# Performance work log

Hardware: AMD Instinct MI355X
Metric: run time of the kernel (lower is better)

Reference implementation:

```python
import jax, jax.numpy as jnp
import numpy as np

B, S, D_MODEL, D_ATTN = 4, 2048, 1024, 1024
NEG_INF = jnp.float32(-jnp.inf)


def setup_inputs() -> dict:
    key = jax.random.key(0)
    ks = jax.random.split(key, 6)
    scale = 1.0 / np.sqrt(D_MODEL)
    return {
        "x": jax.random.normal(ks[0], (B, S, D_MODEL), dtype=jnp.float32),
        "mask": jnp.ones((B, S), dtype=jnp.float32),
        "Wq": jax.random.normal(ks[1], (D_ATTN, D_MODEL), dtype=jnp.float32) * scale,
        "Wk": jax.random.normal(ks[2], (D_ATTN, D_MODEL), dtype=jnp.float32) * scale,
        "Wv": jax.random.normal(ks[3], (D_ATTN, D_MODEL), dtype=jnp.float32) * scale,
        "Wo": jax.random.normal(ks[4], (D_MODEL, D_ATTN), dtype=jnp.float32) * scale,
        "bo": jnp.zeros((D_MODEL,), dtype=jnp.float32),
    }


def reference(x, mask, Wq, Wk, Wv, Wo, bo):
    # x: [B,S,Dm]; torch Linear weight is [out,in], so y = x @ W.T
    q = jnp.einsum("bsd,ad->bsa", x, Wq)  # [B,S,Da]
    k = jnp.einsum("bsd,ad->bsa", x, Wk)
    v = jnp.einsum("bsd,ad->bsa", x, Wv)  # NOTE: v from x (original quirk)
    logits = jnp.einsum("bqa,bka->bqk", q, k)  # [B,S,S]
    # causal mask (cross_attention=True path): keep lower triangle incl. diag
    causal = jnp.tril(jnp.ones((S, S), dtype=bool))
    logits = jnp.where(causal[None], logits, NEG_INF)
    # padding mask: outer product of per-token mask
    square_mask = mask[:, :, None] * mask[:, None, :]  # [B,S,S]
    logits = jnp.where(square_mask == 1, logits, NEG_INF)
    # scale by sqrt(d_model) AFTER masking (as in original)
    attn = jax.nn.softmax(logits / jnp.sqrt(jnp.float32(D_MODEL)), axis=-1)
    attn_out = jnp.einsum("bqk,bka->bqa", attn, v)  # [B,S,Da]
    return jnp.einsum("bsa,da->bsd", attn_out, Wo) + bo
```

## Files before the change

kernel.cpp:

```cpp
#include <hip/hip_runtime.h>
#include <hip/hip_bf16.h>
#include <cstdio>

typedef __bf16 bf16x8 __attribute__((ext_vector_type(8)));
typedef float f32x4 __attribute__((ext_vector_type(4)));

#define BM 128
#define BN 128
#define BK 64

__device__ __forceinline__ unsigned short f2bf(float f) {
  union { float f; unsigned u; } v; v.f = f;
  unsigned u = v.u;
  return (unsigned short)((u + 0x7FFFu + ((u >> 16) & 1u)) >> 16);
}

__device__ __forceinline__ float bf2f(unsigned short s) {
  union { unsigned u; float f; } v; v.u = ((unsigned)s) << 16;
  return v.f;
}

#define GLOAD16(gsrc, ldst) \
  __builtin_amdgcn_global_load_lds((const __attribute__((address_space(1))) void*)(gsrc), \
                                   (__attribute__((address_space(3))) void*)(ldst), 16, 0, 0)

#define SB_KLOOP(Ab, Bb)                                                        \
  for (int kt = 0; kt < 16; kt++) {                                             \
    const unsigned short* Ak = (Ab) + kt * BK;                                  \
    const unsigned short* Bk = (Bb) + kt * BK;                                  \
    _Pragma("unroll")                                                           \
    for (int r = 0; r < 4; r++) {                                               \
      int row = r * 32 + srow;                                                  \
      int sc = sch ^ (row & 7);                                                 \
      GLOAD16(Ak + (long)row * 1024 + sc * 8, &lds[0][(r * 32 + wave * 8) * BK]);\
    }                                                                           \
    _Pragma("unroll")                                                           \
    for (int r = 0; r < 4; r++) {                                               \
      int row = r * 32 + srow;                                                  \
      int sc = sch ^ (row & 7);                                                 \
      GLOAD16(Bk + (long)row * 1024 + sc * 8, &lds[1][(r * 32 + wave * 8) * BK]);\
    }                                                                           \
    __syncthreads();                                                            \
    _Pragma("unroll")                                                           \
    for (int s = 0; s < 2; s++) {                                               \
      bf16x8 av[4], bv[4];                                                      \
      _Pragma("unroll")                                                         \
      for (int i = 0; i < 4; i++) av[i] = *reinterpret_cast<const bf16x8*>(lds[0] + aOff[i][s]); \
      _Pragma("unroll")                                                         \
      for (int j = 0; j < 4; j++) bv[j] = *reinterpret_cast<const bf16x8*>(lds[1] + bOff[j][s]); \
      _Pragma("unroll")                                                         \
      for (int i = 0; i < 4; i++)                                               \
        _Pragma("unroll")                                                       \
        for (int j = 0; j < 4; j++)                                             \
          acc[i][j] = __builtin_amdgcn_mfma_f32_16x16x32_bf16(av[i], bv[j], acc[i][j], 0, 0, 0); \
    }                                                                           \
    __syncthreads();                                                            \
  }

#define SB_PREAMBLE                                                             \
  const int tid = threadIdx.x;                                                  \
  const int lane = tid & 63;                                                    \
  const int wave = tid >> 6;                                                    \
  const int wr = wave >> 1, wc = wave & 1;                                      \
  const int srow = tid >> 3;                                                    \
  const int sch = tid & 7;                                                      \
  (void)srow; (void)sch;                                                        \
  const f32x4 fzero = {0.f, 0.f, 0.f, 0.f};                                     \
  f32x4 acc[4][4];                                                              \
  _Pragma("unroll")                                                             \
  for (int i = 0; i < 4; i++)                                                   \
    _Pragma("unroll")                                                           \
    for (int j = 0; j < 4; j++) acc[i][j] = fzero;                              \
  int aOff[4][2], bOff[4][2];                                                   \
  _Pragma("unroll")                                                             \
  for (int i = 0; i < 4; i++) {                                                 \
    _Pragma("unroll")                                                           \
    for (int s = 0; s < 2; s++) {                                               \
      int ra = wr * 64 + i * 16 + (lane & 15);                                  \
      aOff[i][s] = ra * BK + (((s * 4 + (lane >> 4)) ^ (ra & 7)) * 8);          \
      int rb = wc * 64 + i * 16 + (lane & 15);                                  \
      bOff[i][s] = rb * BK + (((s * 4 + (lane >> 4)) ^ (rb & 7)) * 8);          \
    }                                                                           \
  }

__global__ __launch_bounds__(256)
void cast_ow(const float* __restrict__ Wo, const float* __restrict__ Wv,
             unsigned short* __restrict__ Wob, unsigned short* __restrict__ Wvt)
{
  __shared__ float t[64][65];
  const int blk = blockIdx.x;
  const int tid = threadIdx.x;
  if (blk < 512) {
    const int i = (blk * 256 + tid) * 8;
    float4 a = *reinterpret_cast<const float4*>(Wo + i);
    float4 b = *reinterpret_cast<const float4*>(Wo + i + 4);
    union { unsigned short us[8]; uint4 u4; } pk;
    pk.us[0] = f2bf(a.x); pk.us[1] = f2bf(a.y); pk.us[2] = f2bf(a.z); pk.us[3] = f2bf(a.w);
    pk.us[4] = f2bf(b.x); pk.us[5] = f2bf(b.y); pk.us[6] = f2bf(b.z); pk.us[7] = f2bf(b.w);
    *reinterpret_cast<uint4*>(Wob + i) = pk.u4;
    return;
  }
  const int tile = blk - 512;
  const int a0 = (tile >> 4) * 64;
  const int m0 = (tile & 15) * 64;
#pragma unroll
  for (int i = 0; i < 4; i++) {
    const int row = (tid >> 4) + i * 16;
    const int col4 = tid & 15;
    float4 f4 = *reinterpret_cast<const float4*>(Wv + (long)(a0 + row) * 1024 + m0 + col4 * 4);
    t[row][col4 * 4 + 0] = f4.x;
    t[row][col4 * 4 + 1] = f4.y;
    t[row][col4 * 4 + 2] = f4.z;
    t[row][col4 * 4 + 3] = f4.w;
  }
  __syncthreads();
#pragma unroll
  for (int j = 0; j < 2; j++) {
    const int mm = (tid >> 3) + j * 32;
    const int aa0 = (tid & 7) * 8;
    union { unsigned short us[8]; uint4 u4; } pk;
#pragma unroll
    for (int u = 0; u < 8; u++) pk.us[u] = f2bf(t[aa0 + u][mm]);
    *reinterpret_cast<uint4*>(Wvt + (long)(m0 + mm) * 1024 + a0 + aa0) = pk.u4;
  }
}

__global__ __launch_bounds__(256, 3)
void prep2(const float* __restrict__ x, const float* __restrict__ Wq,
           const float* __restrict__ Wk,
           const unsigned short* __restrict__ Wob, const unsigned short* __restrict__ Wvt,
           unsigned short* __restrict__ xb, unsigned short* __restrict__ Wqk,
           unsigned short* __restrict__ Wvo)
{
  __shared__ short lds[2][BM * BK];
  const int blk = blockIdx.x;

  if (blk >= 64) {
    const int tid = threadIdx.x;
    const float* src;
    unsigned short* dst;
    int i;
    if (blk < 4160) {
      src = x; dst = xb; i = ((blk - 64) * 256 + tid) * 8;
    } else {
      const int w = (blk - 4160) >> 9;
      const int off = (blk - 4160) & 511;
      src = (w == 0) ? Wq : Wk;
      dst = Wqk + (long)w * 1024 * 1024;
      i = (off * 256 + tid) * 8;
    }
    float4 a = *reinterpret_cast<const float4*>(src + i);
    float4 b = *reinterpret_cast<const float4*>(src + i + 4);
    union { unsigned short us[8]; uint4 u4; } pk;
    pk.us[0] = f2bf(a.x); pk.us[1] = f2bf(a.y); pk.us[2] = f2bf(a.z); pk.us[3] = f2bf(a.w);
    pk.us[4] = f2bf(b.x); pk.us[5] = f2bf(b.y); pk.us[6] = f2bf(b.z); pk.us[7] = f2bf(b.w);
    *reinterpret_cast<uint4*>(dst + i) = pk.u4;
    return;
  }

  const int t = blk;
  const int m0 = (t >> 3) * BM, n0 = (t & 7) * BN;
  const unsigned short* Ab = Wob + (long)m0 * 1024;
  const unsigned short* Bb = Wvt + (long)n0 * 1024;

  SB_PREAMBLE
  SB_KLOOP(Ab, Bb)

  const int rb4 = (lane >> 4) * 4;
  const int cl = lane & 15;
#pragma unroll
  for (int i = 0; i < 4; i++) {
#pragma unroll
    for (int j = 0; j < 4; j++) {
      const int gm = m0 + wr * 64 + i * 16 + rb4;
      const int gn = n0 + wc * 64 + j * 16 + cl;
#pragma unroll
      for (int r = 0; r < 4; r++)
        Wvo[(long)(gm + r) * 1024 + gn] = f2bf(acc[i][j][r]);
    }
  }
}

__global__ __launch_bounds__(256, 3)
void dispA2(const unsigned short* __restrict__ Xbf, const unsigned short* __restrict__ Wqk,
            const unsigned short* __restrict__ Wvo,
            unsigned short* __restrict__ Qb, unsigned short* __restrict__ Kb,
            unsigned short* __restrict__ VWt)
{
  __shared__ short lds[2][BM * BK];
  const int flat = blockIdx.x;
  const bool isQK = flat < 1024;
  int m0, n0;
  const unsigned short *Ab, *Bb;
  if (isQK) {
    const int swz = (flat & 7) * 128 + (flat >> 3);
    const int bx = swz & 15, by = swz >> 4;
    m0 = by * BM; n0 = bx * BN;
    Ab = Xbf + (long)m0 * 1024;
    Bb = Wqk + (long)n0 * 1024;
  } else {
    const int t = flat - 1024;
    const int swz = (t & 7) * 64 + (t >> 3);
    const int bx = swz & 7, by = swz >> 3;
    m0 = by * BM; n0 = bx * BN;
    Ab = Xbf + (long)m0 * 1024;
    Bb = Wvo + (long)n0 * 1024;
  }

  SB_PREAMBLE
  SB_KLOOP(Ab, Bb)

  const int rb4 = (lane >> 4) * 4;
  const int cl = lane & 15;
#pragma unroll
  for (int i = 0; i < 4; i++) {
#pragma unroll
    for (int j = 0; j < 4; j++) {
      const int gm = m0 + wr * 64 + i * 16 + rb4;
      const int gn = n0 + wc * 64 + j * 16 + cl;
      if (isQK) {
        if (gn < 1024) {
#pragma unroll
          for (int r = 0; r < 4; r++)
            Qb[(long)(gm + r) * 1024 + gn] = f2bf(acc[i][j][r]);
        } else {
#pragma unroll
          for (int r = 0; r < 4; r++)
            Kb[(long)(gm + r) * 1024 + (gn - 1024)] = f2bf(acc[i][j][r]);
        }
      } else {
        const int b = gm >> 11;
        const int sIdx = gm & 2047;
        unsigned short* C = VWt + (long)b * (2048L * 1024) + (long)gn * 2048 + sIdx;
        ushort4 pk;
        pk.x = f2bf(acc[i][j][0]);
        pk.y = f2bf(acc[i][j][1]);
        pk.z = f2bf(acc[i][j][2]);
        pk.w = f2bf(acc[i][j][3]);
        *reinterpret_cast<ushort4*>(C) = pk;
      }
    }
  }
}

__global__ __launch_bounds__(256, 3)
void dispS(const unsigned short* __restrict__ Qb, const unsigned short* __restrict__ Kb,
           unsigned short* __restrict__ Sb)
{
  __shared__ short lds[2][BM * BK];
  const int t = blockIdx.x;
  const int bz = t / 136;
  const int tt = t - bz * 136;
  const int swz = (tt & 7) * 17 + (tt >> 3);
  int i = (int)((sqrtf(8.f * (float)swz + 1.f) - 1.f) * 0.5f);
  while ((i + 1) * (i + 2) / 2 <= swz) ++i;
  while (i * (i + 1) / 2 > swz) --i;
  const int j = swz - i * (i + 1) / 2;
  const int m0 = i * BM, n0 = j * BN;
  const unsigned short* Ab = Qb + ((long)bz * 2048 + m0) * 1024;
  const unsigned short* Bb = Kb + ((long)bz * 2048 + n0) * 1024;

  SB_PREAMBLE
  SB_KLOOP(Ab, Bb)

  const int rb4 = (lane >> 4) * 4;
  const int cl = lane & 15;
  unsigned short* C = Sb + (long)bz * (2048L * 2048);
#pragma unroll
  for (int ii = 0; ii < 4; ii++) {
#pragma unroll
    for (int jj = 0; jj < 4; jj++) {
      const int gm = m0 + wr * 64 + ii * 16 + rb4;
      const int gn = n0 + wc * 64 + jj * 16 + cl;
#pragma unroll
      for (int r = 0; r < 4; r++)
        C[(long)(gm + r) * 2048 + gn] = f2bf(acc[ii][jj][r] * 0.03125f);
    }
  }
}

__global__ __launch_bounds__(256, 2)
void gemm_pv(const unsigned short* __restrict__ A, const unsigned short* __restrict__ B,
             float* __restrict__ Cv, const float* __restrict__ bias,
             int K, int ldA, int ldB, int ldC,
             long aBat, long bBat, long cBat)
{
  const int gx = gridDim.x;
  const int nwg = gx * gridDim.y;
  const int flat = blockIdx.y * gx + blockIdx.x;
  const int qch = nwg >> 3, rch = nwg & 7;
  const int xcd = flat & 7, idx = flat >> 3;
  const int swz = (xcd < rch ? xcd * (qch + 1) : rch * (qch + 1) + (xcd - rch) * qch) + idx;
  const int bx = swz % gx;
  const int bz = blockIdx.z;
  int by = swz / gx;
  if (bz >= 2) by = gridDim.y - 1 - by;

  const int m0 = by * BM;
  const int n0 = bx * BN;

  const unsigned short* Ab = A + (long)bz * aBat + (long)m0 * ldA;
  const unsigned short* Bb = B + (long)bz * bBat + (long)n0 * ldB;

  __shared__ short lds[2][2][BM * BK];

  const int tid = threadIdx.x;
  const int lane = tid & 63;
  const int wave = tid >> 6;
  const int wr = wave >> 1, wc = wave & 1;

  const int Keff = min(K, m0 + BM);
  const int nk = Keff / BK;

  const int srow = tid >> 3;
  const int sch = tid & 7;

  const f32x4 fzero = {0.f, 0.f, 0.f, 0.f};
  f32x4 acc[4][4];
#pragma unroll
  for (int i = 0; i < 4; i++)
#pragma unroll
    for (int j = 0; j < 4; j++) acc[i][j] = fzero;

  int aOff[4][2], bOff[4][2];
#pragma unroll
  for (int i = 0; i < 4; i++) {
#pragma unroll
    for (int s = 0; s < 2; s++) {
      int ra = wr * 64 + i * 16 + (lane & 15);
      aOff[i][s] = ra * BK + (((s * 4 + (lane >> 4)) ^ (ra & 7)) * 8);
      int rb = wc * 64 + i * 16 + (lane & 15);
      bOff[i][s] = rb * BK + (((s * 4 + (lane >> 4)) ^ (rb & 7)) * 8);
    }
  }

  auto stage = [&](int buf, int kt) {
    const unsigned short* Ak = Ab + kt * BK;
    const unsigned short* Bk = Bb + kt * BK;
#pragma unroll
    for (int r = 0; r < 4; r++) {
      int row = r * 32 + srow;
      int sc = sch ^ (row & 7);
      GLOAD16(Ak + (long)row * ldA + sc * 8, &lds[buf][0][(r * 32 + wave * 8) * BK]);
    }
#pragma unroll
    for (int r = 0; r < 4; r++) {
      int row = r * 32 + srow;
      int sc = sch ^ (row & 7);
      GLOAD16(Bk + (long)row * ldB + sc * 8, &lds[buf][1][(r * 32 + wave * 8) * BK]);
    }
  };

  stage(0, 0);
  stage(1, 1);
  asm volatile("s_waitcnt vmcnt(8)" ::: "memory");
  __builtin_amdgcn_sched_barrier(0);
  __builtin_amdgcn_s_barrier();

  int cur = 0;
  for (int kt = 0; kt < nk; kt++) {
    const short* La = lds[cur][0];
    const short* Lb = lds[cur][1];
    bf16x8 av[2][4], bv[2][4];
#pragma unroll
    for (int s = 0; s < 2; s++) {
#pragma unroll
      for (int i = 0; i < 4; i++) {
        av[s][i] = *reinterpret_cast<const bf16x8*>(La + aOff[i][s]);
        bv[s][i] = *reinterpret_cast<const bf16x8*>(Lb + bOff[i][s]);
      }
    }
    asm volatile("s_waitcnt lgkmcnt(0)" ::: "memory");
    __builtin_amdgcn_sched_barrier(0);
    __builtin_amdgcn_s_barrier();
    __builtin_amdgcn_sched_barrier(0);

    if (kt + 2 < nk) {
      stage(cur, kt + 2);
      asm volatile("s_waitcnt vmcnt(8)" ::: "memory");
    } else if (kt + 1 < nk) {
      asm volatile("s_waitcnt vmcnt(0)" ::: "memory");
    }
    if (kt + 1 < nk) {
      __builtin_amdgcn_s_barrier();
      __builtin_amdgcn_sched_barrier(0);
    }

    __builtin_amdgcn_s_setprio(1);
#pragma unroll
    for (int s = 0; s < 2; s++)
#pragma unroll
      for (int i = 0; i < 4; i++)
#pragma unroll
        for (int j = 0; j < 4; j++)
          acc[i][j] = __builtin_amdgcn_mfma_f32_16x16x32_bf16(av[s][i], bv[s][j], acc[i][j], 0, 0, 0);
    __builtin_amdgcn_s_setprio(0);
    __builtin_amdgcn_sched_barrier(0);
    cur ^= 1;
  }

  const int rb4 = (lane >> 4) * 4;
  const int cl = lane & 15;
#pragma unroll
  for (int i = 0; i < 4; i++) {
#pragma unroll
    for (int j = 0; j < 4; j++) {
      const int gm = m0 + wr * 64 + i * 16 + rb4;
      const int gn = n0 + wc * 64 + j * 16 + cl;
      float* C = Cv + (long)bz * cBat;
      const float bb = bias[gn];
#pragma unroll
      for (int r = 0; r < 4; r++)
        C[(long)(gm + r) * ldC + gn] = acc[i][j][r] + bb;
    }
  }
}

__global__ __launch_bounds__(256)
void softmax_rows(const unsigned short* __restrict__ Sb, const float* __restrict__ maskv,
                  unsigned short* __restrict__ P, int Sdim)
{
  const int wv = threadIdx.x >> 6;
  const int lane = threadIdx.x & 63;
  const int q = blockIdx.x * 4 + wv;
  const int b = blockIdx.y;
  const int kmax = (q & ~127) + 128;
  const unsigned short* row = Sb + ((long)b * Sdim + q) * Sdim;
  unsigned short* prow = P + ((long)b * Sdim + q) * Sdim;
  const float* mrow = maskv + (long)b * Sdim;
  const float mq = mrow[q];

  float v[4][8];
  float mx = -INFINITY;
#pragma unroll
  for (int c = 0; c < 4; c++) {
    const int k0 = c * 512 + lane * 8;
    if (c * 512 < kmax) {
      uint4 raw = *reinterpret_cast<const uint4*>(row + k0);
      const unsigned short* us = reinterpret_cast<const unsigned short*>(&raw);
      float4 ma = *reinterpret_cast<const float4*>(mrow + k0);
      float4 mb = *reinterpret_cast<const float4*>(mrow + k0 + 4);
      float mv[8] = {ma.x, ma.y, ma.z, ma.w, mb.x, mb.y, mb.z, mb.w};
#pragma unroll
      for (int u = 0; u < 8; u++) {
        const int k = k0 + u;
        const bool ok = (k <= q) && (mq * mv[u] == 1.0f);
        v[c][u] = ok ? bf2f(us[u]) : -INFINITY;
        mx = fmaxf(mx, v[c][u]);
      }
    } else {
#pragma unroll
      for (int u = 0; u < 8; u++) v[c][u] = -INFINITY;
    }
  }
#pragma unroll
  for (int o = 32; o; o >>= 1) mx = fmaxf(mx, __shfl_xor(mx, o));

  float sm = 0.f;
#pragma unroll
  for (int c = 0; c < 4; c++)
#pragma unroll
    for (int u = 0; u < 8; u++) {
      v[c][u] = (v[c][u] > -INFINITY) ? __expf(v[c][u] - mx) : 0.f;
      sm += v[c][u];
    }
#pragma unroll
  for (int o = 32; o; o >>= 1) sm += __shfl_xor(sm, o);
  const float inv = 1.0f / sm;

#pragma unroll
  for (int c = 0; c < 4; c++) {
    if (c * 512 < kmax) {
      union { unsigned short us[8]; uint4 u4; } pk;
#pragma unroll
      for (int u = 0; u < 8; u++) pk.us[u] = f2bf(v[c][u] * inv);
      *reinterpret_cast<uint4*>(prow + c * 512 + lane * 8) = pk.u4;
    }
  }
}

extern "C" void kernel_launch(void* const* d_in, const int* in_sizes, int n_in,
                              void* d_out, int out_size, void* d_ws, size_t ws_size,
                              hipStream_t stream)
{
  const int B = 4, S = 2048, D = 1024;
  const float* x  = (const float*)d_in[0];
  const float* mk = (const float*)d_in[1];
  const float* Wq = (const float*)d_in[2];
  const float* Wk = (const float*)d_in[3];
  const float* Wv = (const float*)d_in[4];
  const float* Wo = (const float*)d_in[5];
  const float* bo = (const float*)d_in[6];
  float* out = (float*)d_out;

  char* ws = (char*)d_ws;
  const long MB = 1024L * 1024L;
  unsigned short* Xbf  = (unsigned short*)(ws + 0);
  unsigned short* Qb   = (unsigned short*)(ws + 16 * MB);
  unsigned short* Kb   = (unsigned short*)(ws + 32 * MB);
  unsigned short* VWt  = (unsigned short*)(ws + 48 * MB);
  unsigned short* Wqk  = (unsigned short*)(ws + 64 * MB);
  unsigned short* Wvo  = (unsigned short*)(ws + 68 * MB);
  unsigned short* Wob  = (unsigned short*)(ws + 70 * MB);
  unsigned short* Sbuf = (unsigned short*)(ws + 72 * MB);
  unsigned short* Wvt  = Sbuf;
  unsigned short* P    = Qb;

  if (ws_size < (size_t)(104 * MB)) {
    fprintf(stderr, "kernel_launch: ws too small (%zu bytes, need 104MB)\n", ws_size);
    return;
  }

  cast_ow<<<dim3(768), dim3(256), 0, stream>>>(Wo, Wv, Wob, Wvt);
  prep2<<<dim3(5184), dim3(256), 0, stream>>>(x, Wq, Wk, Wob, Wvt, Xbf, Wqk, Wvo);
  dispA2<<<dim3(1536), dim3(256), 0, stream>>>(Xbf, Wqk, Wvo, Qb, Kb, VWt);
  dispS<<<dim3(544), dim3(256), 0, stream>>>(Qb, Kb, Sbuf);
  softmax_rows<<<dim3(512, 4), dim3(256), 0, stream>>>(Sbuf, mk, P, 2048);
  dim3 gO(1024 / BN, 2048 / BM, 4);
  gemm_pv<<<gO, dim3(256), 0, stream>>>(P, VWt, out, bo,
                                        2048, 2048, 2048, 1024,
                                        (long)S * S, (long)D * S, (long)S * D);
}
```

Before: 155.9 us.

## Fuse softmax into score epilogue and normalize inside the PV GEMM

The score GEMM epilogue now applies the causal and padding masks and writes exp(score/32) directly. This removes the separate row-softmax kernel and its full read and write pass over the score matrix. The PV GEMM computes row sums with extra MFMAs against a ones vector and divides by them in its epilogue. In exchange the max subtraction is dropped, so large logits could overflow, and the PV GEMM does about a quarter more MFMA work.

```diff
diff --git a/kernel.cpp b/kernel.cpp
--- a/kernel.cpp
+++ b/kernel.cpp
@@ -13,11 +13,6 @@
   union { float f; unsigned u; } v; v.f = f;
   unsigned u = v.u;
   return (unsigned short)((u + 0x7FFFu + ((u >> 16) & 1u)) >> 16);
-}
-
-__device__ __forceinline__ float bf2f(unsigned short s) {
-  union { unsigned u; float f; } v; v.u = ((unsigned)s) << 16;
-  return v.f;
 }
 
 #define GLOAD16(gsrc, ldst) \
@@ -245,7 +240,7 @@
 
 __global__ __launch_bounds__(256, 3)
 void dispS(const unsigned short* __restrict__ Qb, const unsigned short* __restrict__ Kb,
-           unsigned short* __restrict__ Sb)
+           const float* __restrict__ mk, unsigned short* __restrict__ Eb)
 {
   __shared__ short lds[2][BM * BK];
   const int t = blockIdx.x;
@@ -265,16 +260,22 @@
 
   const int rb4 = (lane >> 4) * 4;
   const int cl = lane & 15;
-  unsigned short* C = Sb + (long)bz * (2048L * 2048);
+  unsigned short* C = Eb + (long)bz * (2048L * 2048);
+  const float* mrow = mk + (long)bz * 2048;
 #pragma unroll
   for (int ii = 0; ii < 4; ii++) {
 #pragma unroll
     for (int jj = 0; jj < 4; jj++) {
       const int gm = m0 + wr * 64 + ii * 16 + rb4;
       const int gn = n0 + wc * 64 + jj * 16 + cl;
-#pragma unroll
-      for (int r = 0; r < 4; r++)
-        C[(long)(gm + r) * 2048 + gn] = f2bf(acc[ii][jj][r] * 0.03125f);
+      const float mv = mrow[gn];
+#pragma unroll
+      for (int r = 0; r < 4; r++) {
+        const int row = gm + r;
+        const bool ok = (gn <= row) && (mrow[row] * mv == 1.0f);
+        const float e = ok ? __expf(acc[ii][jj][r] * 0.03125f) : 0.f;
+        C[(long)row * 2048 + gn] = f2bf(e);
+      }
     }
   }
 }
@@ -317,10 +318,16 @@
 
   const f32x4 fzero = {0.f, 0.f, 0.f, 0.f};
   f32x4 acc[4][4];
-#pragma unroll
-  for (int i = 0; i < 4; i++)
+  f32x4 accs[4];
+#pragma unroll
+  for (int i = 0; i < 4; i++) {
+    accs[i] = fzero;
 #pragma unroll
     for (int j = 0; j < 4; j++) acc[i][j] = fzero;
+  }
+  bf16x8 vone;
+#pragma unroll
+  for (int u = 0; u < 8; u++) vone[u] = (__bf16)1.0f;
 
   int aOff[4][2], bOff[4][2];
 #pragma unroll
@@ -388,12 +395,16 @@
 
     __builtin_amdgcn_s_setprio(1);
 #pragma unroll
-    for (int s = 0; s < 2; s++)
+    for (int s = 0; s < 2; s++) {
 #pragma unroll
       for (int i = 0; i < 4; i++)
 #pragma unroll
         for (int j = 0; j < 4; j++)
           acc[i][j] = __builtin_amdgcn_mfma_f32_16x16x32_bf16(av[s][i], bv[s][j], acc[i][j], 0, 0, 0);
+#pragma unroll
+      for (int i = 0; i < 4; i++)
+        accs[i] = __builtin_amdgcn_mfma_f32_16x16x32_bf16(av[s][i], vone, accs[i], 0, 0, 0);
+    }
     __builtin_amdgcn_s_setprio(0);
     __builtin_amdgcn_sched_barrier(0);
     cur ^= 1;
@@ -403,6 +414,9 @@
   const int cl = lane & 15;
 #pragma unroll
   for (int i = 0; i < 4; i++) {
+    float invr[4];
+#pragma unroll
+    for (int r = 0; r < 4; r++) invr[r] = 1.0f / accs[i][r];
 #pragma unroll
     for (int j = 0; j < 4; j++) {
       const int gm = m0 + wr * 64 + i * 16 + rb4;
@@ -411,70 +425,7 @@
       const float bb = bias[gn];
 #pragma unroll
       for (int r = 0; r < 4; r++)
-        C[(long)(gm + r) * ldC + gn] = acc[i][j][r] + bb;
-    }
-  }
-}
-
-__global__ __launch_bounds__(256)
-void softmax_rows(const unsigned short* __restrict__ Sb, const float* __restrict__ maskv,
-                  unsigned short* __restrict__ P, int Sdim)
-{
-  const int wv = threadIdx.x >> 6;
-  const int lane = threadIdx.x & 63;
-  const int q = blockIdx.x * 4 + wv;
-  const int b = blockIdx.y;
-  const int kmax = (q & ~127) + 128;
-  const unsigned short* row = Sb + ((long)b * Sdim + q) * Sdim;
-  unsigned short* prow = P + ((long)b * Sdim + q) * Sdim;
-  const float* mrow = maskv + (long)b * Sdim;
-  const float mq = mrow[q];
-
-  float v[4][8];
-  float mx = -INFINITY;
-#pragma unroll
-  for (int c = 0; c < 4; c++) {
-    const int k0 = c * 512 + lane * 8;
-    if (c * 512 < kmax) {
-      uint4 raw = *reinterpret_cast<const uint4*>(row + k0);
-      const unsigned short* us = reinterpret_cast<const unsigned short*>(&raw);
-      float4 ma = *reinterpret_cast<const float4*>(mrow + k0);
-      float4 mb = *reinterpret_cast<const float4*>(mrow + k0 + 4);
-      float mv[8] = {ma.x, ma.y, ma.z, ma.w, mb.x, mb.y, mb.z, mb.w};
-#pragma unroll
-      for (int u = 0; u < 8; u++) {
-        const int k = k0 + u;
-        const bool ok = (k <= q) && (mq * mv[u] == 1.0f);
-        v[c][u] = ok ? bf2f(us[u]) : -INFINITY;
-        mx = fmaxf(mx, v[c][u]);
-      }
-    } else {
-#pragma unroll
-      for (int u = 0; u < 8; u++) v[c][u] = -INFINITY;
-    }
-  }
-#pragma unroll
-  for (int o = 32; o; o >>= 1) mx = fmaxf(mx, __shfl_xor(mx, o));
-
-  float sm = 0.f;
-#pragma unroll
-  for (int c = 0; c < 4; c++)
-#pragma unroll
-    for (int u = 0; u < 8; u++) {
-      v[c][u] = (v[c][u] > -INFINITY) ? __expf(v[c][u] - mx) : 0.f;
-      sm += v[c][u];
-    }
-#pragma unroll
-  for (int o = 32; o; o >>= 1) sm += __shfl_xor(sm, o);
-  const float inv = 1.0f / sm;
-
-#pragma unroll
-  for (int c = 0; c < 4; c++) {
-    if (c * 512 < kmax) {
-      union { unsigned short us[8]; uint4 u4; } pk;
-#pragma unroll
-      for (int u = 0; u < 8; u++) pk.us[u] = f2bf(v[c][u] * inv);
-      *reinterpret_cast<uint4*>(prow + c * 512 + lane * 8) = pk.u4;
+        C[(long)(gm + r) * ldC + gn] = acc[i][j][r] * invr[r] + bb;
     }
   }
 }
@@ -502,9 +453,8 @@
   unsigned short* Wqk  = (unsigned short*)(ws + 64 * MB);
   unsigned short* Wvo  = (unsigned short*)(ws + 68 * MB);
   unsigned short* Wob  = (unsigned short*)(ws + 70 * MB);
-  unsigned short* Sbuf = (unsigned short*)(ws + 72 * MB);
-  unsigned short* Wvt  = Sbuf;
-  unsigned short* P    = Qb;
+  unsigned short* Ebuf = (unsigned short*)(ws + 72 * MB);
+  unsigned short* Wvt  = Ebuf;
 
   if (ws_size < (size_t)(104 * MB)) {
     fprintf(stderr, "kernel_launch: ws too small (%zu bytes, need 104MB)\n", ws_size);
@@ -514,10 +464,9 @@
   cast_ow<<<dim3(768), dim3(256), 0, stream>>>(Wo, Wv, Wob, Wvt);
   prep2<<<dim3(5184), dim3(256), 0, stream>>>(x, Wq, Wk, Wob, Wvt, Xbf, Wqk, Wvo);
   dispA2<<<dim3(1536), dim3(256), 0, stream>>>(Xbf, Wqk, Wvo, Qb, Kb, VWt);
-  dispS<<<dim3(544), dim3(256), 0, stream>>>(Qb, Kb, Sbuf);
-  softmax_rows<<<dim3(512, 4), dim3(256), 0, stream>>>(Sbuf, mk, P, 2048);
+  dispS<<<dim3(544), dim3(256), 0, stream>>>(Qb, Kb, mk, Ebuf);
   dim3 gO(1024 / BN, 2048 / BM, 4);
-  gemm_pv<<<gO, dim3(256), 0, stream>>>(P, VWt, out, bo,
+  gemm_pv<<<gO, dim3(256), 0, stream>>>(Ebuf, VWt, out, bo,
                                         2048, 2048, 2048, 1024,
                                         (long)S * S, (long)D * S, (long)S * D);
 }
```

Result: faster. 151.7 us (-2.7%).
